# Optimization experiments

Measured on AMD Instinct MI355X. Metric: run time of the kernel, lower is better.

Reference implementation:

```python
import jax, jax.numpy as jnp
import numpy as np


def setup_inputs() -> dict:
    key = jax.random.key(0)
    k1, k2, k3, k4 = jax.random.split(key, 4)
    I, Q, P, S, N = 512000, 128, 1, 8, 4000
    x = jax.random.normal(k1, (I, Q), dtype=jnp.float32)
    beta_u = jax.random.normal(k2, (Q, P, S), dtype=jnp.float32)
    beta_z = jax.random.normal(k3, (Q, P, S), dtype=jnp.float32)
    i = jnp.sort(jax.random.randint(k4, (I,), 0, N, dtype=jnp.int64))
    return {"x": x, "beta_u": beta_u, "beta_z": beta_z, "i": i, "n_bags": N}


def _scatter_softmax(u, seg, num_segments):
    # numerically stable softmax over variable-size segments (bags)
    seg_max = jax.ops.segment_max(u, seg, num_segments=num_segments)  # [N,P,S]
    e = jnp.exp(u - seg_max[seg])                                     # [I,P,S]
    denom = jax.ops.segment_sum(e, seg, num_segments=num_segments)    # [N,P,S]
    return e / denom[seg]


def reference(x, beta_u, beta_z, i, n_bags):
    # b = rms of beta_z over latent dim -> [1,P,S]; eta = normalized beta_z
    b = jnp.sqrt(jnp.mean(beta_z ** 2, axis=0, keepdims=True))
    eta = beta_z / b
    # gather -> per-instance projections -> scatter softmax -> segment pooling
    u = jnp.einsum('iq,qps->ips', x, beta_u)      # [I,P,S]
    w = _scatter_softmax(u, i, n_bags)            # [I,P,S]
    z = jnp.einsum('iq,qps->ips', x, eta)         # [I,P,S]
    xmil = jax.ops.segment_sum(w * z, i, num_segments=n_bags)  # [N,P,S]
    # normalize across bags (torch .std is unbiased, ddof=1), rescale by b
    mean = jnp.mean(xmil, axis=0)
    std = jnp.std(xmil, axis=0, ddof=1)
    return b * (xmil - mean) / std
```

## Files before the change

kernel.cpp:

```cpp
#include <hip/hip_runtime.h>
#include <hip/hip_bf16.h>


#define QDIM 128
#define C8 8

typedef __attribute__((ext_vector_type(8))) short s8v;
typedef __attribute__((ext_vector_type(4))) float f4v;

__device__ __forceinline__ void split8(const float xs[8], s8v& AH, s8v& AL) {
#pragma unroll
    for (int j = 0; j < 8; ++j) {
        const float xv = xs[j];
        const __hip_bfloat16 hb = __float2bfloat16(xv);
        const float hf = __bfloat162float(hb);
        const __hip_bfloat16 lb = __float2bfloat16(xv - hf);
        unsigned short hr, lr;
        __builtin_memcpy(&hr, &hb, 2);
        __builtin_memcpy(&lr, &lb, 2);
        AH[j] = (short)hr;
        AL[j] = (short)lr;
    }
}

__global__ __launch_bounds__(256) void mixmil_fused(
    const float* __restrict__ x,
    const float* __restrict__ bu,
    const float* __restrict__ bz,
    const int*   __restrict__ seg,
    int I, int N, int bstride,
    float* __restrict__ xmil)
{
    __shared__ float XT[4 * 2 * 2048];

    const int t    = threadIdx.x;
    const int lane = t & 63;
    const int wv   = t >> 6;

    const int b0 = blockIdx.x * 4 + wv;
    const int b1 = b0 + bstride;
    if (b0 >= N) return;

    int jq = N;
    if (lane == 0) jq = b0;
    else if (lane == 1) jq = b0 + 1;
    else if (lane == 2) jq = (b1 < N) ? b1 : N;
    else if (lane == 3) jq = (b1 + 1 < N) ? (b1 + 1) : N;
    int slo = 0, shi = I;
    while (slo < shi) {
        const int mid = (slo + shi) >> 1;
        if (seg[mid] < jq) slo = mid + 1; else shi = mid;
    }
    const int lo0 = __shfl(slo, 0);
    const int hi0 = __shfl(slo, 1);
    int lo1 = 0, hi1 = 0;
    if (b1 < N) { lo1 = __shfl(slo, 2); hi1 = __shfl(slo, 3); }

    const int nt0 = (hi0 - lo0 + 15) >> 4;
    const int nt1 = (hi1 - lo1 + 15) >> 4;
    const int total = nt0 + nt1;

    if (lane < 8) {
        if (nt0 == 0) xmil[(size_t)b0 * 8 + lane] = 0.f;
        if (b1 < N && nt1 == 0) xmil[(size_t)b1 * 8 + lane] = 0.f;
    }
    if (total == 0) return;

    const int bn  = lane & 15;
    const int bkg = lane >> 4;
    s8v BH[4], BL[4];
    const float* wcol = (bn < 8) ? (bu + bn) : (bz + (bn - 8));
#pragma unroll
    for (int kc = 0; kc < 4; ++kc) {
        float ws[8];
#pragma unroll
        for (int j = 0; j < 8; ++j)
            ws[j] = wcol[(size_t)(kc * 32 + bkg * 8 + j) * 8];
        split8(ws, BH[kc], BL[kc]);
    }

    float* const myXT = &XT[wv * 4096];
    const int rl  = lane >> 5;
    const int c4l = lane & 31;

#define CH_BASE(C) (((C) >= nt0) ? (lo1 + (((C) - nt0) << 4)) : (lo0 + ((C) << 4)))
#define CH_LIM(C)  (((C) >= nt0) ? hi1 : hi0)

#define STAGE(C)                                                               \
    {                                                                          \
        const int base_ = CH_BASE(C);                                          \
        const int lim_  = CH_LIM(C);                                           \
        float* dst_ = &myXT[((C) & 1) * 2048];                                 \
        _Pragma("unroll")                                                      \
        for (int i = 0; i < 8; ++i) {                                          \
            const int r_ = i * 2 + rl;                                         \
            int grow_ = base_ + r_;                                            \
            if (grow_ >= lim_) grow_ = lim_ - 1;                               \
            const int c4g_ = c4l ^ (r_ & 7);                                   \
            const float* src_ = x + (size_t)grow_ * QDIM + 4 * (size_t)c4g_;   \
            __builtin_amdgcn_global_load_lds(                                  \
                (const __attribute__((address_space(1))) unsigned int*)src_,   \
                (__attribute__((address_space(3))) unsigned int*)              \
                    (dst_ + i * 256),                                          \
                16, 0, 0);                                                     \
        }                                                                      \
    }

    float lsum = 0.f, asum = 0.f;

    const int am  = lane & 15;
    const int akg = lane >> 4;
    const int sw  = am & 7;

    STAGE(0);

    for (int c = 0; c < total; ++c) {
        if (c + 1 < total) {
            STAGE(c + 1);
            asm volatile("s_waitcnt vmcnt(8)" ::: "memory");
        } else {
            asm volatile("s_waitcnt vmcnt(0)" ::: "memory");
        }
        __builtin_amdgcn_sched_barrier(0);

        const float* buf = &myXT[(c & 1) * 2048];

        f4v acc = {0.f, 0.f, 0.f, 0.f};
#pragma unroll
        for (int kc = 0; kc < 4; ++kc) {
            const int c4a = kc * 8 + akg * 2;
            const float4 xa = *(const float4*)&buf[am * QDIM + 4 * ((c4a    ) ^ sw)];
            const float4 xb = *(const float4*)&buf[am * QDIM + 4 * ((c4a + 1) ^ sw)];
            const float xs[8] = {xa.x, xa.y, xa.z, xa.w, xb.x, xb.y, xb.z, xb.w};
            s8v AH, AL;
            split8(xs, AH, AL);
            acc = __builtin_amdgcn_mfma_f32_16x16x32_bf16(AH, BH[kc], acc, 0, 0, 0);
            acc = __builtin_amdgcn_mfma_f32_16x16x32_bf16(AH, BL[kc], acc, 0, 0, 0);
            acc = __builtin_amdgcn_mfma_f32_16x16x32_bf16(AL, BH[kc], acc, 0, 0, 0);
        }

        const int base = CH_BASE(c);
        const int lim  = CH_LIM(c);
        const int r0   = (lane >> 4) * 4;
#pragma unroll
        for (int i = 0; i < 4; ++i) {
            const float uv = acc[i];
            const float zv = __shfl_xor(uv, 8);
            const bool valid = (base + r0 + i) < lim;
            if ((lane & 15) < 8 && valid) {
                const float e = __expf(uv);
                lsum += e;
                asum = fmaf(e, zv, asum);
            }
        }

        const bool fin0 = (c == nt0 - 1);
        const bool fin1 = (c == total - 1) && (nt1 > 0);
        if (fin0 || fin1) {
            float ls = lsum, as = asum;
            ls += __shfl_xor(ls, 16);
            as += __shfl_xor(as, 16);
            ls += __shfl_xor(ls, 32);
            as += __shfl_xor(as, 32);
            const int bag = fin0 ? b0 : b1;
            if (lane < 8)
                xmil[(size_t)bag * 8 + lane] = as / ls;
            lsum = 0.f; asum = 0.f;
        }
    }
#undef STAGE
#undef CH_BASE
#undef CH_LIM
}

__global__ __launch_bounds__(256) void mixmil_statsout(
    const float* __restrict__ xmil,
    const float* __restrict__ bz,
    int N, int total,
    float* __restrict__ out)
{
    double s[8], qq[8];
    float t2[8];
#pragma unroll
    for (int c = 0; c < 8; ++c) { s[c] = 0.0; qq[c] = 0.0; t2[c] = 0.f; }

    for (int r = threadIdx.x; r < N; r += 256) {
        const float* row = xmil + (size_t)r * 8;
#pragma unroll
        for (int c = 0; c < 8; ++c) {
            float v = row[c];
            s[c] += v;
            qq[c] += (double)v * (double)v;
        }
    }
    for (int r = threadIdx.x; r < QDIM; r += 256) {
        const float* row = bz + (size_t)r * 8;
#pragma unroll
        for (int c = 0; c < 8; ++c) { float v = row[c]; t2[c] = fmaf(v, v, t2[c]); }
    }

    for (int off = 32; off; off >>= 1) {
#pragma unroll
        for (int c = 0; c < 8; ++c) {
            s[c]  += __shfl_xor(s[c], off);
            qq[c] += __shfl_xor(qq[c], off);
            t2[c] += __shfl_xor(t2[c], off);
        }
    }

    __shared__ double S[4][8], QQ[4][8];
    __shared__ float T2[4][8];
    __shared__ float fb[8], fm[8], fr[8];
    const int w = threadIdx.x >> 6;
    if ((threadIdx.x & 63) == 0) {
#pragma unroll
        for (int c = 0; c < 8; ++c) { S[w][c] = s[c]; QQ[w][c] = qq[c]; T2[w][c] = t2[c]; }
    }
    __syncthreads();
    if (threadIdx.x < 8) {
        const int c = threadIdx.x;
        double ss = S[0][c] + S[1][c] + S[2][c] + S[3][c];
        double qs = QQ[0][c] + QQ[1][c] + QQ[2][c] + QQ[3][c];
        float  tt = T2[0][c] + T2[1][c] + T2[2][c] + T2[3][c];
        double mean = ss / (double)N;
        double var  = (qs - ss * ss / (double)N) / (double)(N - 1);
        fb[c] = sqrtf(tt / (float)QDIM);
        fm[c] = (float)mean;
        fr[c] = (float)(1.0 / sqrt(var));
    }
    __syncthreads();

    const int e = blockIdx.x * 256 + threadIdx.x;
    if (e < total) {
        const int c = e & 7;
        out[e] = fb[c] * (xmil[e] - fm[c]) * fr[c];
    }
}

extern "C" void kernel_launch(void* const* d_in, const int* in_sizes, int n_in,
                              void* d_out, int out_size, void* d_ws, size_t ws_size,
                              hipStream_t stream) {
    const float* x  = (const float*)d_in[0];
    const float* bu = (const float*)d_in[1];
    const float* bz = (const float*)d_in[2];
    const int*   sg = (const int*)d_in[3];

    const int I = in_sizes[0] / QDIM;
    const int N = out_size / C8;

    const int nblk = (N + 7) / 8;
    const int bstride = nblk * 4;

    float* xmil = (float*)d_ws;

    mixmil_fused<<<nblk, 256, 0, stream>>>(x, bu, bz, sg, I, N, bstride, xmil);

    const int total = N * C8;
    mixmil_statsout<<<(total + 255) / 256, 256, 0, stream>>>(
        xmil, bz, N, total, (float*)d_out);
}
```

Baseline: 60.78 us.

## Fuse stats/normalize kernel into main kernel via last-block atomic counter

Removes the second kernel launch. Each block increments a global counter after finishing its bags, and the last block to arrive computes the column mean, std and rms and writes the normalized output. This saves a launch and its gap, but adds a memset of the counter and leaves the final pass over 32K elements to a single block, serialized at the tail.

```diff
diff --git a/kernel.cpp b/kernel.cpp
--- a/kernel.cpp
+++ b/kernel.cpp
@@ -29,7 +29,9 @@
     const float* __restrict__ bz,
     const int*   __restrict__ seg,
     int I, int N, int bstride,
-    float* __restrict__ xmil)
+    float* __restrict__ xmil,
+    int*   __restrict__ counter,
+    float* __restrict__ out)
 {
     __shared__ float XT[4 * 2 * 2048];
 
@@ -39,7 +41,6 @@
 
     const int b0 = blockIdx.x * 4 + wv;
     const int b1 = b0 + bstride;
-    if (b0 >= N) return;
 
     int jq = N;
     if (lane == 0) jq = b0;
@@ -64,127 +65,132 @@
         if (nt0 == 0) xmil[(size_t)b0 * 8 + lane] = 0.f;
         if (b1 < N && nt1 == 0) xmil[(size_t)b1 * 8 + lane] = 0.f;
     }
-    if (total == 0) return;
-
-    const int bn  = lane & 15;
-    const int bkg = lane >> 4;
-    s8v BH[4], BL[4];
-    const float* wcol = (bn < 8) ? (bu + bn) : (bz + (bn - 8));
-#pragma unroll
-    for (int kc = 0; kc < 4; ++kc) {
-        float ws[8];
-#pragma unroll
-        for (int j = 0; j < 8; ++j)
-            ws[j] = wcol[(size_t)(kc * 32 + bkg * 8 + j) * 8];
-        split8(ws, BH[kc], BL[kc]);
-    }
-
-    float* const myXT = &XT[wv * 4096];
-    const int rl  = lane >> 5;
-    const int c4l = lane & 31;
+
+    if (total > 0) {
+        const int bn  = lane & 15;
+        const int bkg = lane >> 4;
+        s8v BH[4], BL[4];
+        const float* wcol = (bn < 8) ? (bu + bn) : (bz + (bn - 8));
+#pragma unroll
+        for (int kc = 0; kc < 4; ++kc) {
+            float ws[8];
+#pragma unroll
+            for (int j = 0; j < 8; ++j)
+                ws[j] = wcol[(size_t)(kc * 32 + bkg * 8 + j) * 8];
+            split8(ws, BH[kc], BL[kc]);
+        }
+
+        float* const myXT = &XT[wv * 4096];
+        const int rl  = lane >> 5;
+        const int c4l = lane & 31;
 
 #define CH_BASE(C) (((C) >= nt0) ? (lo1 + (((C) - nt0) << 4)) : (lo0 + ((C) << 4)))
 #define CH_LIM(C)  (((C) >= nt0) ? hi1 : hi0)
 
 #define STAGE(C)                                                               \
-    {                                                                          \
-        const int base_ = CH_BASE(C);                                          \
-        const int lim_  = CH_LIM(C);                                           \
-        float* dst_ = &myXT[((C) & 1) * 2048];                                 \
-        _Pragma("unroll")                                                      \
-        for (int i = 0; i < 8; ++i) {                                          \
-            const int r_ = i * 2 + rl;                                         \
-            int grow_ = base_ + r_;                                            \
-            if (grow_ >= lim_) grow_ = lim_ - 1;                               \
-            const int c4g_ = c4l ^ (r_ & 7);                                   \
-            const float* src_ = x + (size_t)grow_ * QDIM + 4 * (size_t)c4g_;   \
-            __builtin_amdgcn_global_load_lds(                                  \
-                (const __attribute__((address_space(1))) unsigned int*)src_,   \
-                (__attribute__((address_space(3))) unsigned int*)              \
-                    (dst_ + i * 256),                                          \
-                16, 0, 0);                                                     \
-        }                                                                      \
-    }
-
-    float lsum = 0.f, asum = 0.f;
-
-    const int am  = lane & 15;
-    const int akg = lane >> 4;
-    const int sw  = am & 7;
-
-    STAGE(0);
-
-    for (int c = 0; c < total; ++c) {
-        if (c + 1 < total) {
-            STAGE(c + 1);
-            asm volatile("s_waitcnt vmcnt(8)" ::: "memory");
-        } else {
-            asm volatile("s_waitcnt vmcnt(0)" ::: "memory");
-        }
-        __builtin_amdgcn_sched_barrier(0);
-
-        const float* buf = &myXT[(c & 1) * 2048];
-
-        f4v acc = {0.f, 0.f, 0.f, 0.f};
-#pragma unroll
-        for (int kc = 0; kc < 4; ++kc) {
-            const int c4a = kc * 8 + akg * 2;
-            const float4 xa = *(const float4*)&buf[am * QDIM + 4 * ((c4a    ) ^ sw)];
-            const float4 xb = *(const float4*)&buf[am * QDIM + 4 * ((c4a + 1) ^ sw)];
-            const float xs[8] = {xa.x, xa.y, xa.z, xa.w, xb.x, xb.y, xb.z, xb.w};
-            s8v AH, AL;
-            split8(xs, AH, AL);
-            acc = __builtin_amdgcn_mfma_f32_16x16x32_bf16(AH, BH[kc], acc, 0, 0, 0);
-            acc = __builtin_amdgcn_mfma_f32_16x16x32_bf16(AH, BL[kc], acc, 0, 0, 0);
-            acc = __builtin_amdgcn_mfma_f32_16x16x32_bf16(AL, BH[kc], acc, 0, 0, 0);
-        }
-
-        const int base = CH_BASE(c);
-        const int lim  = CH_LIM(c);
-        const int r0   = (lane >> 4) * 4;
-#pragma unroll
-        for (int i = 0; i < 4; ++i) {
-            const float uv = acc[i];
-            const float zv = __shfl_xor(uv, 8);
-            const bool valid = (base + r0 + i) < lim;
-            if ((lane & 15) < 8 && valid) {
-                const float e = __expf(uv);
-                lsum += e;
-                asum = fmaf(e, zv, asum);
-            }
-        }
-
-        const bool fin0 = (c == nt0 - 1);
-        const bool fin1 = (c == total - 1) && (nt1 > 0);
-        if (fin0 || fin1) {
-            float ls = lsum, as = asum;
-            ls += __shfl_xor(ls, 16);
-            as += __shfl_xor(as, 16);
-            ls += __shfl_xor(ls, 32);
-            as += __shfl_xor(as, 32);
-            const int bag = fin0 ? b0 : b1;
-            if (lane < 8)
-                xmil[(size_t)bag * 8 + lane] = as / ls;
-            lsum = 0.f; asum = 0.f;
-        }
-    }
+        {                                                                      \
+            const int base_ = CH_BASE(C);                                      \
+            const int lim_  = CH_LIM(C);                                       \
+            float* dst_ = &myXT[((C) & 1) * 2048];                             \
+            _Pragma("unroll")                                                  \
+            for (int i = 0; i < 8; ++i) {                                      \
+                const int r_ = i * 2 + rl;                                     \
+                int grow_ = base_ + r_;                                        \
+                if (grow_ >= lim_) grow_ = lim_ - 1;                           \
+                const int c4g_ = c4l ^ (r_ & 7);                               \
+                const float* src_ = x + (size_t)grow_ * QDIM + 4 * (size_t)c4g_; \
+                __builtin_amdgcn_global_load_lds(                              \
+                    (const __attribute__((address_space(1))) unsigned int*)src_, \
+                    (__attribute__((address_space(3))) unsigned int*)          \
+                        (dst_ + i * 256),                                      \
+                    16, 0, 0);                                                 \
+            }                                                                  \
+        }
+
+        float lsum = 0.f, asum = 0.f;
+
+        const int am  = lane & 15;
+        const int akg = lane >> 4;
+        const int sw  = am & 7;
+
+        STAGE(0);
+
+        for (int c = 0; c < total; ++c) {
+            if (c + 1 < total) {
+                STAGE(c + 1);
+                asm volatile("s_waitcnt vmcnt(8)" ::: "memory");
+            } else {
+                asm volatile("s_waitcnt vmcnt(0)" ::: "memory");
+            }
+            __builtin_amdgcn_sched_barrier(0);
+
+            const float* buf = &myXT[(c & 1) * 2048];
+
+            f4v acc = {0.f, 0.f, 0.f, 0.f};
+#pragma unroll
+            for (int kc = 0; kc < 4; ++kc) {
+                const int c4a = kc * 8 + akg * 2;
+                const float4 xa = *(const float4*)&buf[am * QDIM + 4 * ((c4a    ) ^ sw)];
+                const float4 xb = *(const float4*)&buf[am * QDIM + 4 * ((c4a + 1) ^ sw)];
+                const float xs[8] = {xa.x, xa.y, xa.z, xa.w, xb.x, xb.y, xb.z, xb.w};
+                s8v AH, AL;
+                split8(xs, AH, AL);
+                acc = __builtin_amdgcn_mfma_f32_16x16x32_bf16(AH, BH[kc], acc, 0, 0, 0);
+                acc = __builtin_amdgcn_mfma_f32_16x16x32_bf16(AH, BL[kc], acc, 0, 0, 0);
+                acc = __builtin_amdgcn_mfma_f32_16x16x32_bf16(AL, BH[kc], acc, 0, 0, 0);
+            }
+
+            const int base = CH_BASE(c);
+            const int lim  = CH_LIM(c);
+            const int r0   = (lane >> 4) * 4;
+#pragma unroll
+            for (int i = 0; i < 4; ++i) {
+                const float uv = acc[i];
+                const float zv = __shfl_xor(uv, 8);
+                const bool valid = (base + r0 + i) < lim;
+                if ((lane & 15) < 8 && valid) {
+                    const float e = __expf(uv);
+                    lsum += e;
+                    asum = fmaf(e, zv, asum);
+                }
+            }
+
+            const bool fin0 = (c == nt0 - 1);
+            const bool fin1 = (c == total - 1) && (nt1 > 0);
+            if (fin0 || fin1) {
+                float ls = lsum, as = asum;
+                ls += __shfl_xor(ls, 16);
+                as += __shfl_xor(as, 16);
+                ls += __shfl_xor(ls, 32);
+                as += __shfl_xor(as, 32);
+                const int bag = fin0 ? b0 : b1;
+                if (lane < 8)
+                    xmil[(size_t)bag * 8 + lane] = as / ls;
+                lsum = 0.f; asum = 0.f;
+            }
+        }
 #undef STAGE
 #undef CH_BASE
 #undef CH_LIM
-}
-
-__global__ __launch_bounds__(256) void mixmil_statsout(
-    const float* __restrict__ xmil,
-    const float* __restrict__ bz,
-    int N, int total,
-    float* __restrict__ out)
-{
+    }
+
+    __shared__ int isLast;
+    __syncthreads();
+    if (t == 0) {
+        __threadfence();
+        const int old = atomicAdd(counter, 1);
+        isLast = (old == (int)gridDim.x - 1) ? 1 : 0;
+    }
+    __syncthreads();
+    if (!isLast) return;
+    __threadfence();
+
     double s[8], qq[8];
     float t2[8];
 #pragma unroll
     for (int c = 0; c < 8; ++c) { s[c] = 0.0; qq[c] = 0.0; t2[c] = 0.f; }
 
-    for (int r = threadIdx.x; r < N; r += 256) {
+    for (int r = t; r < N; r += 256) {
         const float* row = xmil + (size_t)r * 8;
 #pragma unroll
         for (int c = 0; c < 8; ++c) {
@@ -193,7 +199,7 @@
             qq[c] += (double)v * (double)v;
         }
     }
-    for (int r = threadIdx.x; r < QDIM; r += 256) {
+    for (int r = t; r < QDIM; r += 256) {
         const float* row = bz + (size_t)r * 8;
 #pragma unroll
         for (int c = 0; c < 8; ++c) { float v = row[c]; t2[c] = fmaf(v, v, t2[c]); }
@@ -211,14 +217,14 @@
     __shared__ double S[4][8], QQ[4][8];
     __shared__ float T2[4][8];
     __shared__ float fb[8], fm[8], fr[8];
-    const int w = threadIdx.x >> 6;
-    if ((threadIdx.x & 63) == 0) {
+    const int w = t >> 6;
+    if ((t & 63) == 0) {
 #pragma unroll
         for (int c = 0; c < 8; ++c) { S[w][c] = s[c]; QQ[w][c] = qq[c]; T2[w][c] = t2[c]; }
     }
     __syncthreads();
-    if (threadIdx.x < 8) {
-        const int c = threadIdx.x;
+    if (t < 8) {
+        const int c = t;
         double ss = S[0][c] + S[1][c] + S[2][c] + S[3][c];
         double qs = QQ[0][c] + QQ[1][c] + QQ[2][c] + QQ[3][c];
         float  tt = T2[0][c] + T2[1][c] + T2[2][c] + T2[3][c];
@@ -230,8 +236,8 @@
     }
     __syncthreads();
 
-    const int e = blockIdx.x * 256 + threadIdx.x;
-    if (e < total) {
+    const int tot = N * C8;
+    for (int e = t; e < tot; e += 256) {
         const int c = e & 7;
         out[e] = fb[c] * (xmil[e] - fm[c]) * fr[c];
     }
@@ -251,11 +257,11 @@
     const int nblk = (N + 7) / 8;
     const int bstride = nblk * 4;
 
-    float* xmil = (float*)d_ws;
-
-    mixmil_fused<<<nblk, 256, 0, stream>>>(x, bu, bz, sg, I, N, bstride, xmil);
-
-    const int total = N * C8;
-    mixmil_statsout<<<(total + 255) / 256, 256, 0, stream>>>(
-        xmil, bz, N, total, (float*)d_out);
+    float* xmil    = (float*)d_ws;
+    int*   counter = (int*)(xmil + (size_t)N * C8);
+
+    hipMemsetAsync(counter, 0, sizeof(int), stream);
+
+    mixmil_fused<<<nblk, 256, 0, stream>>>(x, bu, bz, sg, I, N, bstride,
+                                           xmil, counter, (float*)d_out);
 }
```

Result: slower. 87.56 us (+44.1%).
